# Optimization experiments

Hardware: AMD Instinct MI355X
Metric: run time of the kernel (lower is better)

## Reference

```python
import jax, jax.numpy as jnp
import numpy as np

FEAT_DIM = 2048
HID = 256
N = 1024
NUM_CLASSES = 16
BN_EPS = 1e-5


def _batchnorm(x, gamma, beta):
    # training-mode BatchNorm1d: per-batch mean, biased variance
    m = x.mean(axis=0)
    v = x.var(axis=0)
    return gamma * (x - m) / jnp.sqrt(v + BN_EPS) + beta


def setup_inputs() -> dict:
    key = jax.random.key(0)
    ks = jax.random.split(key, 12)
    s1 = 1.0 / np.sqrt(FEAT_DIM)
    s2 = 1.0 / np.sqrt(HID)
    s3 = 1.0 / np.sqrt(2 * HID)
    return {
        "features": jax.random.normal(ks[0], (N, FEAT_DIM), dtype=jnp.float32),
        "labels": jax.random.randint(ks[1], (N,), 0, NUM_CLASSES, dtype=jnp.int32),
        # semantic disentangler
        "W1": jax.random.normal(ks[2], (FEAT_DIM, HID), dtype=jnp.float32) * s1,
        "b1": jnp.zeros((HID,), jnp.float32),
        "g1": jnp.ones((HID,), jnp.float32),
        "bt1": jnp.zeros((HID,), jnp.float32),
        "W2": jax.random.normal(ks[3], (HID, HID), dtype=jnp.float32) * s2,
        "b2": jnp.zeros((HID,), jnp.float32),
        "g2": jnp.ones((HID,), jnp.float32),
        "bt2": jnp.zeros((HID,), jnp.float32),
        # edge network: Linear(2H -> H), Linear(H -> 1)
        "We1": jax.random.normal(ks[4], (2 * HID, HID), dtype=jnp.float32) * s3,
        "bwe1": jnp.zeros((HID,), jnp.float32),
        "We2": jax.random.normal(ks[5], (HID, 1), dtype=jnp.float32) * s2,
        "bwe2": jnp.zeros((1,), jnp.float32),
    }


def reference(features, labels, W1, b1, g1, bt1, W2, b2, g2, bt2,
              We1, bwe1, We2, bwe2):
    # semantic disentangler: (Linear -> BN -> ReLU) x2
    h = jax.nn.relu(_batchnorm(features @ W1 + b1, g1, bt1))
    di = jax.nn.relu(_batchnorm(h @ W2 + b2, g2, bt2))  # [N, H]

    # EdgeNetwork all-pairs: Linear on concat([f_i, f_j]) splits into two GEMMs
    hi = di @ We1[:HID]   # [N, H] contribution of node i (first half of concat)
    hj = di @ We1[HID:]   # [N, H] contribution of node j (second half)
    pair = jax.nn.relu(hi[:, None, :] + hj[None, :, :] + bwe1)  # [N, N, H]
    logits = pair @ We2[:, 0] + bwe2[0]                          # [N, N]
    same_label = labels[:, None] == labels[None, :]
    off_diag = ~jnp.eye(N, dtype=bool)
    edge_weights = jnp.where(same_label & off_diag,
                             jax.nn.sigmoid(logits), 0.0)        # [N, N]

    # update_node_features: f_i + sum_j w_ij f_j / sum_j w_ij (if wsum > 0)
    weighted_sum = edge_weights @ di                 # [N, H] (w_ii == 0)
    wsum = edge_weights.sum(axis=1, keepdims=True)   # [N, 1]
    denom = jnp.where(wsum > 0, wsum, 1.0)
    updated = di + jnp.where(wsum > 0, weighted_sum / denom, 0.0)
    return updated
```

## Files before the change

### kernel.cpp

```cpp
#include <hip/hip_runtime.h>
#include <math.h>

#define N_PTS 1024
#define HID   256
#define FEAT  2048

typedef short bf16x8 __attribute__((ext_vector_type(8)));
typedef float f32x4  __attribute__((ext_vector_type(4)));

__device__ inline ushort f2bf(float f) {
    union { float f; unsigned u; } v; v.f = f;
    unsigned r = v.u + 0x7fff + ((v.u >> 16) & 1);
    return (ushort)(r >> 16);
}

__global__ __launch_bounds__(256) void gemm_mfma(
    const float* __restrict__ A, const float* __restrict__ B,
    float* __restrict__ C, int lda, int ldb, int ldc, int kchunk)
{
    __shared__ ushort As[64 * 72];
    __shared__ ushort Bs[64 * 72];
    const int tid  = threadIdx.x;
    const int lane = tid & 63;
    const int wave = tid >> 6;
    const int wy = wave >> 1, wx = wave & 1;
    const int quad = lane >> 4, l16 = lane & 15;
    const int mBase = blockIdx.y * 64;
    const int nBase = blockIdx.x * 64;
    const int kBeg  = blockIdx.z * kchunk;

    f32x4 acc[2][2] = {};

    for (int ks = kBeg; ks < kBeg + kchunk; ks += 64) {
        #pragma unroll
        for (int p = 0; p < 4; p++) {
            const int c  = p * 256 + tid;
            const int r  = c >> 4;
            const int cq = c & 15;
            float4 av = *(const float4*)&A[(size_t)(mBase + r) * lda + ks + cq * 4];
            ushort4 ao;
            ao.x = f2bf(av.x); ao.y = f2bf(av.y);
            ao.z = f2bf(av.z); ao.w = f2bf(av.w);
            *(ushort4*)&As[r * 72 + cq * 4] = ao;
            float4 bv = *(const float4*)&B[(size_t)(ks + r) * ldb + nBase + cq * 4];
            Bs[(cq * 4 + 0) * 72 + r] = f2bf(bv.x);
            Bs[(cq * 4 + 1) * 72 + r] = f2bf(bv.y);
            Bs[(cq * 4 + 2) * 72 + r] = f2bf(bv.z);
            Bs[(cq * 4 + 3) * 72 + r] = f2bf(bv.w);
        }
        __syncthreads();
        #pragma unroll
        for (int kt = 0; kt < 64; kt += 32) {
            bf16x8 af[2], bfr[2];
            #pragma unroll
            for (int mi = 0; mi < 2; mi++)
                af[mi] = *(bf16x8*)&As[(wy * 32 + mi * 16 + l16) * 72 + kt + quad * 8];
            #pragma unroll
            for (int ni = 0; ni < 2; ni++)
                bfr[ni] = *(bf16x8*)&Bs[(wx * 32 + ni * 16 + l16) * 72 + kt + quad * 8];
            #pragma unroll
            for (int mi = 0; mi < 2; mi++)
                #pragma unroll
                for (int ni = 0; ni < 2; ni++)
                    acc[mi][ni] = __builtin_amdgcn_mfma_f32_16x16x32_bf16(
                        af[mi], bfr[ni], acc[mi][ni], 0, 0, 0);
        }
        __syncthreads();
    }
    #pragma unroll
    for (int mi = 0; mi < 2; mi++)
        #pragma unroll
        for (int ni = 0; ni < 2; ni++)
            #pragma unroll
            for (int e = 0; e < 4; e++) {
                const int gm = mBase + wy * 32 + mi * 16 + quad * 4 + e;
                const int gn = nBase + wx * 32 + ni * 16 + l16;
                unsafeAtomicAdd(&C[(size_t)gm * ldc + gn], acc[mi][ni][e]);
            }
}

__global__ __launch_bounds__(256) void colstats(
    const float* __restrict__ X, float* __restrict__ sum,
    float* __restrict__ sq, int rowsPerBlock)
{
    const int c = threadIdx.x;
    const int r0 = blockIdx.x * rowsPerBlock;
    float s = 0.f, q = 0.f;
    for (int r = r0; r < r0 + rowsPerBlock; ++r) {
        float v = X[r * HID + c];
        s += v;
        q = fmaf(v, v, q);
    }
    unsafeAtomicAdd(&sum[c], s);
    unsafeAtomicAdd(&sq[c], q);
}

__global__ __launch_bounds__(256) void bn_relu(
    const float* __restrict__ X, const float* __restrict__ sum,
    const float* __restrict__ sq, const float* __restrict__ g,
    const float* __restrict__ bt, float* __restrict__ Y)
{
    const int idx = blockIdx.x * 256 + threadIdx.x;
    const int cq = (idx & 63) * 4;
    float4 x = ((const float4*)X)[idx];
    float xv[4] = {x.x, x.y, x.z, x.w};
    float o[4];
    #pragma unroll
    for (int e = 0; e < 4; e++) {
        const int c = cq + e;
        float m   = sum[c] * (1.f / 1024.f);
        float var = fmaf(-m, m, sq[c] * (1.f / 1024.f));
        float rstd = rsqrtf(var + 1e-5f);
        o[e] = fmaxf(fmaf(g[c] * rstd, xv[e] - m, bt[c]), 0.f);
    }
    ((float4*)Y)[idx] = make_float4(o[0], o[1], o[2], o[3]);
}

__global__ __launch_bounds__(256) void gemm2_fused(
    const float* __restrict__ A , const float* __restrict__ B ,
    float* __restrict__ C ,
    const float* __restrict__ sum1, const float* __restrict__ sq1,
    const float* __restrict__ g1, const float* __restrict__ bt1,
    float* __restrict__ sum2, float* __restrict__ sq2)
{
    __shared__ ushort As[64 * 72];
    __shared__ ushort Bs[64 * 72];
    __shared__ float sscale[HID];
    __shared__ float sshift[HID];
    __shared__ float csum[64];
    __shared__ float csq[64];
    const int tid  = threadIdx.x;
    const int lane = tid & 63;
    const int wave = tid >> 6;
    const int wy = wave >> 1, wx = wave & 1;
    const int quad = lane >> 4, l16 = lane & 15;
    const int mBase = blockIdx.y * 64;
    const int nBase = blockIdx.x * 64;

    {
        float m   = sum1[tid] * (1.f / 1024.f);
        float var = fmaf(-m, m, sq1[tid] * (1.f / 1024.f));
        float rstd = rsqrtf(var + 1e-5f);
        float sc = g1[tid] * rstd;
        sscale[tid] = sc;
        sshift[tid] = fmaf(-m, sc, bt1[tid]);
    }
    if (tid < 64) { csum[tid] = 0.f; csq[tid] = 0.f; }
    __syncthreads();

    f32x4 acc[2][2] = {};
    for (int ks = 0; ks < HID; ks += 64) {
        #pragma unroll
        for (int p = 0; p < 4; p++) {
            const int c  = p * 256 + tid;
            const int r  = c >> 4;
            const int cq = c & 15;
            const int k0 = ks + cq * 4;
            float4 av = *(const float4*)&A[(size_t)(mBase + r) * HID + k0];
            float v0 = fmaxf(fmaf(sscale[k0 + 0], av.x, sshift[k0 + 0]), 0.f);
            float v1 = fmaxf(fmaf(sscale[k0 + 1], av.y, sshift[k0 + 1]), 0.f);
            float v2 = fmaxf(fmaf(sscale[k0 + 2], av.z, sshift[k0 + 2]), 0.f);
            float v3 = fmaxf(fmaf(sscale[k0 + 3], av.w, sshift[k0 + 3]), 0.f);
            ushort4 ao;
            ao.x = f2bf(v0); ao.y = f2bf(v1); ao.z = f2bf(v2); ao.w = f2bf(v3);
            *(ushort4*)&As[r * 72 + cq * 4] = ao;
            float4 bv = *(const float4*)&B[(size_t)(ks + r) * HID + nBase + cq * 4];
            Bs[(cq * 4 + 0) * 72 + r] = f2bf(bv.x);
            Bs[(cq * 4 + 1) * 72 + r] = f2bf(bv.y);
            Bs[(cq * 4 + 2) * 72 + r] = f2bf(bv.z);
            Bs[(cq * 4 + 3) * 72 + r] = f2bf(bv.w);
        }
        __syncthreads();
        #pragma unroll
        for (int kt = 0; kt < 64; kt += 32) {
            bf16x8 af[2], bfr[2];
            #pragma unroll
            for (int mi = 0; mi < 2; mi++)
                af[mi] = *(bf16x8*)&As[(wy * 32 + mi * 16 + l16) * 72 + kt + quad * 8];
            #pragma unroll
            for (int ni = 0; ni < 2; ni++)
                bfr[ni] = *(bf16x8*)&Bs[(wx * 32 + ni * 16 + l16) * 72 + kt + quad * 8];
            #pragma unroll
            for (int mi = 0; mi < 2; mi++)
                #pragma unroll
                for (int ni = 0; ni < 2; ni++)
                    acc[mi][ni] = __builtin_amdgcn_mfma_f32_16x16x32_bf16(
                        af[mi], bfr[ni], acc[mi][ni], 0, 0, 0);
        }
        __syncthreads();
    }

    float s[2] = {0.f, 0.f}, q[2] = {0.f, 0.f};
    #pragma unroll
    for (int mi = 0; mi < 2; mi++)
        #pragma unroll
        for (int ni = 0; ni < 2; ni++)
            #pragma unroll
            for (int e = 0; e < 4; e++) {
                const int gm = mBase + wy * 32 + mi * 16 + quad * 4 + e;
                const int gn = nBase + wx * 32 + ni * 16 + l16;
                float v = acc[mi][ni][e];
                C[(size_t)gm * HID + gn] = v;
                s[ni] += v;
                q[ni] = fmaf(v, v, q[ni]);
            }
    #pragma unroll
    for (int ni = 0; ni < 2; ni++) {
        float sv = s[ni], qv = q[ni];
        sv += __shfl_xor(sv, 16, 64); sv += __shfl_xor(sv, 32, 64);
        qv += __shfl_xor(qv, 16, 64); qv += __shfl_xor(qv, 32, 64);
        if (quad == 0) {
            atomicAdd(&csum[wx * 32 + ni * 16 + l16], sv);
            atomicAdd(&csq [wx * 32 + ni * 16 + l16], qv);
        }
    }
    __syncthreads();
    if (tid < 64) {
        unsafeAtomicAdd(&sum2[nBase + tid], csum[tid]);
        unsafeAtomicAdd(&sq2 [nBase + tid], csq[tid]);
    }
}

__global__ __launch_bounds__(256) void gemm_dual(
    const float* __restrict__ A, const float* __restrict__ B1,
    const float* __restrict__ B2, float* __restrict__ C1, float* __restrict__ C2)
{
    __shared__ ushort As[64 * 72];
    __shared__ ushort Bs[64 * 72];
    const int tid  = threadIdx.x;
    const int lane = tid & 63;
    const int wave = tid >> 6;
    const int wy = wave >> 1, wx = wave & 1;
    const int quad = lane >> 4, l16 = lane & 15;
    const int mBase = blockIdx.y * 64;
    const int nBase = blockIdx.x * 64;
    const float* B = (blockIdx.z >= 4) ? B2 : B1;
    float*       C = (blockIdx.z >= 4) ? C2 : C1;
    const int ks = (blockIdx.z & 3) * 64;

    f32x4 acc[2][2] = {};
    #pragma unroll
    for (int p = 0; p < 4; p++) {
        const int c  = p * 256 + tid;
        const int r  = c >> 4;
        const int cq = c & 15;
        float4 av = *(const float4*)&A[(size_t)(mBase + r) * HID + ks + cq * 4];
        ushort4 ao;
        ao.x = f2bf(av.x); ao.y = f2bf(av.y);
        ao.z = f2bf(av.z); ao.w = f2bf(av.w);
        *(ushort4*)&As[r * 72 + cq * 4] = ao;
        float4 bv = *(const float4*)&B[(size_t)(ks + r) * HID + nBase + cq * 4];
        Bs[(cq * 4 + 0) * 72 + r] = f2bf(bv.x);
        Bs[(cq * 4 + 1) * 72 + r] = f2bf(bv.y);
        Bs[(cq * 4 + 2) * 72 + r] = f2bf(bv.z);
        Bs[(cq * 4 + 3) * 72 + r] = f2bf(bv.w);
    }
    __syncthreads();
    #pragma unroll
    for (int kt = 0; kt < 64; kt += 32) {
        bf16x8 af[2], bfr[2];
        #pragma unroll
        for (int mi = 0; mi < 2; mi++)
            af[mi] = *(bf16x8*)&As[(wy * 32 + mi * 16 + l16) * 72 + kt + quad * 8];
        #pragma unroll
        for (int ni = 0; ni < 2; ni++)
            bfr[ni] = *(bf16x8*)&Bs[(wx * 32 + ni * 16 + l16) * 72 + kt + quad * 8];
        #pragma unroll
        for (int mi = 0; mi < 2; mi++)
            #pragma unroll
            for (int ni = 0; ni < 2; ni++)
                acc[mi][ni] = __builtin_amdgcn_mfma_f32_16x16x32_bf16(
                    af[mi], bfr[ni], acc[mi][ni], 0, 0, 0);
    }
    #pragma unroll
    for (int mi = 0; mi < 2; mi++)
        #pragma unroll
        for (int ni = 0; ni < 2; ni++)
            #pragma unroll
            for (int e = 0; e < 4; e++) {
                const int gm = mBase + wy * 32 + mi * 16 + quad * 4 + e;
                const int gn = nBase + wx * 32 + ni * 16 + l16;
                unsafeAtomicAdd(&C[(size_t)gm * HID + gn], acc[mi][ni][e]);
            }
}

__global__ __launch_bounds__(256) void pair_update2(
    const float* __restrict__ di, const float* __restrict__ hi,
    const float* __restrict__ hj, const float* __restrict__ bwe1,
    const float* __restrict__ We2, const float* __restrict__ bwe2,
    const int* __restrict__ labels, float* __restrict__ out)
{
    __shared__ int   slab[N_PTS];
    __shared__ int   list[N_PTS];
    __shared__ int   cnt;
    __shared__ float sacc[16][HID];
    __shared__ float swsum[16];
    const int i   = blockIdx.x;
    const int tid = threadIdx.x;
    const int pid = tid >> 4;
    const int l16 = tid & 15;

    if (tid == 0) cnt = 0;
    for (int t = tid; t < N_PTS; t += 256) slab[t] = labels[t];
    __syncthreads();
    const int myLab = slab[i];
    for (int t = tid; t < N_PTS; t += 256)
        if (slab[t] == myLab && t != i) list[atomicAdd(&cnt, 1)] = t;
    __syncthreads();
    const int n = cnt;

    const float4* hip4 = (const float4*)(hi + (size_t)i * HID) + l16 * 4;
    const float4* bw4  = (const float4*)bwe1 + l16 * 4;
    const float4* w24  = (const float4*)We2  + l16 * 4;
    float4 hb[4], w2[4];
    #pragma unroll
    for (int s = 0; s < 4; s++) {
        float4 a = hip4[s], b = bw4[s];
        hb[s] = make_float4(a.x + b.x, a.y + b.y, a.z + b.z, a.w + b.w);
        w2[s] = w24[s];
    }
    const float b2 = bwe2[0];

    float4 acc[4] = {};
    float wloc = 0.f;
    const int rounds = (n + 15) >> 4;
    for (int r = 0; r < rounds; ++r) {
        const int idx = r * 16 + pid;
        const bool valid = idx < n;
        const int jj = valid ? list[idx] : i;
        const float4* hv4 = (const float4*)(hj + (size_t)jj * HID) + l16 * 4;
        float4 hv[4];
        #pragma unroll
        for (int s = 0; s < 4; s++) hv[s] = hv4[s];
        float p = 0.f;
        #pragma unroll
        for (int s = 0; s < 4; s++) {
            p = fmaf(fmaxf(hb[s].x + hv[s].x, 0.f), w2[s].x, p);
            p = fmaf(fmaxf(hb[s].y + hv[s].y, 0.f), w2[s].y, p);
            p = fmaf(fmaxf(hb[s].z + hv[s].z, 0.f), w2[s].z, p);
            p = fmaf(fmaxf(hb[s].w + hv[s].w, 0.f), w2[s].w, p);
        }
        p += __shfl_xor(p, 1, 64);
        p += __shfl_xor(p, 2, 64);
        p += __shfl_xor(p, 4, 64);
        p += __shfl_xor(p, 8, 64);
        const float w = valid ? 1.f / (1.f + expf(-(p + b2))) : 0.f;
        const float4* dv4 = (const float4*)(di + (size_t)jj * HID) + l16 * 4;
        #pragma unroll
        for (int s = 0; s < 4; s++) {
            float4 d = dv4[s];
            acc[s].x = fmaf(w, d.x, acc[s].x);
            acc[s].y = fmaf(w, d.y, acc[s].y);
            acc[s].z = fmaf(w, d.z, acc[s].z);
            acc[s].w = fmaf(w, d.w, acc[s].w);
        }
        if (l16 == 0) wloc += w;
    }
    #pragma unroll
    for (int s = 0; s < 4; s++)
        ((float4*)&sacc[pid][l16 * 16])[s] = acc[s];
    if (l16 == 0) swsum[pid] = wloc;
    __syncthreads();

    float at = 0.f;
    #pragma unroll
    for (int g = 0; g < 16; g++) at += sacc[g][tid];
    float wt = 0.f;
    #pragma unroll
    for (int g = 0; g < 16; g++) wt += swsum[g];
    const float dval = di[(size_t)i * HID + tid];
    out[(size_t)i * HID + tid] = dval + (wt > 0.f ? at / wt : 0.f);
}

extern "C" void kernel_launch(void* const* d_in, const int* in_sizes, int n_in,
                              void* d_out, int out_size, void* d_ws, size_t ws_size,
                              hipStream_t stream)
{
    const float* features = (const float*)d_in[0];
    const int*   labels   = (const int*)d_in[1];
    const float* W1   = (const float*)d_in[2];
    const float* g1   = (const float*)d_in[4];
    const float* bt1  = (const float*)d_in[5];
    const float* W2   = (const float*)d_in[6];
    const float* g2   = (const float*)d_in[8];
    const float* bt2  = (const float*)d_in[9];
    const float* We1  = (const float*)d_in[10];
    const float* bwe1 = (const float*)d_in[11];
    const float* We2  = (const float*)d_in[12];
    const float* bwe2 = (const float*)d_in[13];
    float* out = (float*)d_out;

    float* ws    = (float*)d_ws;
    float* x1    = ws;
    float* hi    = ws + 262144;
    float* hj    = ws + 524288;
    float* stats = ws + 786432;
    float* x2    = ws + 787456;
    float* di    = ws + 1049600;

    hipMemsetAsync(d_ws, 0, 787456 * sizeof(float), stream);

    dim3 blk(256);
    gemm_mfma<<<dim3(4, 16, 8), blk, 0, stream>>>(features, W1, x1,
                                                  FEAT, HID, HID, 256);
    colstats<<<256, blk, 0, stream>>>(x1, stats, stats + 256, 4);
    gemm2_fused<<<dim3(4, 16, 1), blk, 0, stream>>>(x1, W2, x2,
                                                    stats, stats + 256, g1, bt1,
                                                    stats + 512, stats + 768);
    bn_relu<<<256, blk, 0, stream>>>(x2, stats + 512, stats + 768, g2, bt2, di);
    gemm_dual<<<dim3(4, 16, 8), blk, 0, stream>>>(di, We1, We1 + HID * HID,
                                                  hi, hj);
    pair_update2<<<N_PTS, blk, 0, stream>>>(di, hi, hj, bwe1, We2, bwe2,
                                            labels, out);
}
```

Before: 155.1 us.

## Pre-convert inputs and weights to transposed bf16 and fuse BN2 into dual GEMM

```diff
diff --git a/kernel.cpp b/kernel.cpp
--- a/kernel.cpp
+++ b/kernel.cpp
@@ -14,8 +14,61 @@
     return (ushort)(r >> 16);
 }
 
-__global__ __launch_bounds__(256) void gemm_mfma(
-    const float* __restrict__ A, const float* __restrict__ B,
+__global__ __launch_bounds__(256) void prep(
+    const float* __restrict__ features, const float* __restrict__ W1,
+    const float* __restrict__ W2, const float* __restrict__ We1,
+    ushort* __restrict__ Af, ushort* __restrict__ W1T,
+    ushort* __restrict__ W2T, ushort* __restrict__ WeT)
+{
+    const int tid = threadIdx.x;
+    int b = blockIdx.x;
+    if (b < 512) {
+        #pragma unroll
+        for (int q = 0; q < 2; q++) {
+            const size_t g = (size_t)b * 256 + tid + (size_t)q * 131072;
+            float4 v0 = ((const float4*)features)[g * 2];
+            float4 v1 = ((const float4*)features)[g * 2 + 1];
+            bf16x8 o;
+            o[0] = (short)f2bf(v0.x); o[1] = (short)f2bf(v0.y);
+            o[2] = (short)f2bf(v0.z); o[3] = (short)f2bf(v0.w);
+            o[4] = (short)f2bf(v1.x); o[5] = (short)f2bf(v1.y);
+            o[6] = (short)f2bf(v1.z); o[7] = (short)f2bf(v1.w);
+            ((bf16x8*)Af)[g] = o;
+        }
+        return;
+    }
+    __shared__ ushort Ts[64 * 72];
+    const float* src; ushort* dst; int K;
+    b -= 512;
+    if (b < 128)      { src = W1;  dst = W1T; K = 2048; }
+    else if (b < 144) { b -= 128; src = W2;  dst = W2T; K = 256; }
+    else              { b -= 144; src = We1; dst = WeT; K = 512; }
+    const int k0 = (b >> 2) * 64;
+    const int n0 = (b & 3) * 64;
+    #pragma unroll
+    for (int p = 0; p < 4; p++) {
+        const int c  = p * 256 + tid;
+        const int r  = c >> 4;
+        const int cq = c & 15;
+        float4 v = *(const float4*)&src[(size_t)(k0 + r) * 256 + n0 + cq * 4];
+        Ts[(cq * 4 + 0) * 72 + r] = f2bf(v.x);
+        Ts[(cq * 4 + 1) * 72 + r] = f2bf(v.y);
+        Ts[(cq * 4 + 2) * 72 + r] = f2bf(v.z);
+        Ts[(cq * 4 + 3) * 72 + r] = f2bf(v.w);
+    }
+    __syncthreads();
+    #pragma unroll
+    for (int p = 0; p < 2; p++) {
+        const int c    = p * 256 + tid;
+        const int row  = c >> 3;
+        const int col8 = c & 7;
+        *(bf16x8*)&dst[(size_t)(n0 + row) * K + k0 + col8 * 8] =
+            *(bf16x8*)&Ts[row * 72 + col8 * 8];
+    }
+}
+
+__global__ __launch_bounds__(256) void gemm_bf(
+    const ushort* __restrict__ A, const ushort* __restrict__ B,
     float* __restrict__ C, int lda, int ldb, int ldc, int kchunk)
 {
     __shared__ ushort As[64 * 72];
@@ -30,23 +83,16 @@
     const int kBeg  = blockIdx.z * kchunk;
 
     f32x4 acc[2][2] = {};
-
     for (int ks = kBeg; ks < kBeg + kchunk; ks += 64) {
         #pragma unroll
-        for (int p = 0; p < 4; p++) {
-            const int c  = p * 256 + tid;
-            const int r  = c >> 4;
-            const int cq = c & 15;
-            float4 av = *(const float4*)&A[(size_t)(mBase + r) * lda + ks + cq * 4];
-            ushort4 ao;
-            ao.x = f2bf(av.x); ao.y = f2bf(av.y);
-            ao.z = f2bf(av.z); ao.w = f2bf(av.w);
-            *(ushort4*)&As[r * 72 + cq * 4] = ao;
-            float4 bv = *(const float4*)&B[(size_t)(ks + r) * ldb + nBase + cq * 4];
-            Bs[(cq * 4 + 0) * 72 + r] = f2bf(bv.x);
-            Bs[(cq * 4 + 1) * 72 + r] = f2bf(bv.y);
-            Bs[(cq * 4 + 2) * 72 + r] = f2bf(bv.z);
-            Bs[(cq * 4 + 3) * 72 + r] = f2bf(bv.w);
+        for (int p = 0; p < 2; p++) {
+            const int c    = p * 256 + tid;
+            const int row  = c >> 3;
+            const int col8 = c & 7;
+            *(bf16x8*)&As[row * 72 + col8 * 8] =
+                *(const bf16x8*)&A[(size_t)(mBase + row) * lda + ks + col8 * 8];
+            *(bf16x8*)&Bs[row * 72 + col8 * 8] =
+                *(const bf16x8*)&B[(size_t)(nBase + row) * ldb + ks + col8 * 8];
         }
         __syncthreads();
         #pragma unroll
@@ -95,29 +141,8 @@
     unsafeAtomicAdd(&sq[c], q);
 }
 
-__global__ __launch_bounds__(256) void bn_relu(
-    const float* __restrict__ X, const float* __restrict__ sum,
-    const float* __restrict__ sq, const float* __restrict__ g,
-    const float* __restrict__ bt, float* __restrict__ Y)
-{
-    const int idx = blockIdx.x * 256 + threadIdx.x;
-    const int cq = (idx & 63) * 4;
-    float4 x = ((const float4*)X)[idx];
-    float xv[4] = {x.x, x.y, x.z, x.w};
-    float o[4];
-    #pragma unroll
-    for (int e = 0; e < 4; e++) {
-        const int c = cq + e;
-        float m   = sum[c] * (1.f / 1024.f);
-        float var = fmaf(-m, m, sq[c] * (1.f / 1024.f));
-        float rstd = rsqrtf(var + 1e-5f);
-        o[e] = fmaxf(fmaf(g[c] * rstd, xv[e] - m, bt[c]), 0.f);
-    }
-    ((float4*)Y)[idx] = make_float4(o[0], o[1], o[2], o[3]);
-}
-
 __global__ __launch_bounds__(256) void gemm2_fused(
-    const float* __restrict__ A , const float* __restrict__ B ,
+    const float* __restrict__ A , const ushort* __restrict__ B ,
     float* __restrict__ C ,
     const float* __restrict__ sum1, const float* __restrict__ sq1,
     const float* __restrict__ g1, const float* __restrict__ bt1,
@@ -164,11 +189,14 @@
             ushort4 ao;
             ao.x = f2bf(v0); ao.y = f2bf(v1); ao.z = f2bf(v2); ao.w = f2bf(v3);
             *(ushort4*)&As[r * 72 + cq * 4] = ao;
-            float4 bv = *(const float4*)&B[(size_t)(ks + r) * HID + nBase + cq * 4];
-            Bs[(cq * 4 + 0) * 72 + r] = f2bf(bv.x);
-            Bs[(cq * 4 + 1) * 72 + r] = f2bf(bv.y);
-            Bs[(cq * 4 + 2) * 72 + r] = f2bf(bv.z);
-            Bs[(cq * 4 + 3) * 72 + r] = f2bf(bv.w);
+        }
+        #pragma unroll
+        for (int p = 0; p < 2; p++) {
+            const int c    = p * 256 + tid;
+            const int row  = c >> 3;
+            const int col8 = c & 7;
+            *(bf16x8*)&Bs[row * 72 + col8 * 8] =
+                *(const bf16x8*)&B[(size_t)(nBase + row) * HID + ks + col8 * 8];
         }
         __syncthreads();
         #pragma unroll
@@ -221,12 +249,17 @@
     }
 }
 
-__global__ __launch_bounds__(256) void gemm_dual(
-    const float* __restrict__ A, const float* __restrict__ B1,
-    const float* __restrict__ B2, float* __restrict__ C1, float* __restrict__ C2)
+__global__ __launch_bounds__(256) void gemm_dual_bn(
+    const float* __restrict__ A , const ushort* __restrict__ WeT,
+    float* __restrict__ C1 , float* __restrict__ C2 ,
+    const float* __restrict__ sum2, const float* __restrict__ sq2,
+    const float* __restrict__ g2, const float* __restrict__ bt2,
+    float* __restrict__ di)
 {
     __shared__ ushort As[64 * 72];
     __shared__ ushort Bs[64 * 72];
+    __shared__ float sscale[HID];
+    __shared__ float sshift[HID];
     const int tid  = threadIdx.x;
     const int lane = tid & 63;
     const int wave = tid >> 6;
@@ -234,28 +267,50 @@
     const int quad = lane >> 4, l16 = lane & 15;
     const int mBase = blockIdx.y * 64;
     const int nBase = blockIdx.x * 64;
-    const float* B = (blockIdx.z >= 4) ? B2 : B1;
-    float*       C = (blockIdx.z >= 4) ? C2 : C1;
-    const int ks = (blockIdx.z & 3) * 64;
-
-    f32x4 acc[2][2] = {};
+    const int half  = blockIdx.z >> 2;
+    const int ks    = (blockIdx.z & 3) * 64;
+    float* C = half ? C2 : C1;
+    const bool writeDi = (blockIdx.x == 0) && (half == 0);
+
+    {
+        float m   = sum2[tid] * (1.f / 1024.f);
+        float var = fmaf(-m, m, sq2[tid] * (1.f / 1024.f));
+        float rstd = rsqrtf(var + 1e-5f);
+        float sc = g2[tid] * rstd;
+        sscale[tid] = sc;
+        sshift[tid] = fmaf(-m, sc, bt2[tid]);
+    }
+    __syncthreads();
+
     #pragma unroll
     for (int p = 0; p < 4; p++) {
         const int c  = p * 256 + tid;
         const int r  = c >> 4;
         const int cq = c & 15;
-        float4 av = *(const float4*)&A[(size_t)(mBase + r) * HID + ks + cq * 4];
+        const int k0 = ks + cq * 4;
+        float4 av = *(const float4*)&A[(size_t)(mBase + r) * HID + k0];
+        float v0 = fmaxf(fmaf(sscale[k0 + 0], av.x, sshift[k0 + 0]), 0.f);
+        float v1 = fmaxf(fmaf(sscale[k0 + 1], av.y, sshift[k0 + 1]), 0.f);
+        float v2 = fmaxf(fmaf(sscale[k0 + 2], av.z, sshift[k0 + 2]), 0.f);
+        float v3 = fmaxf(fmaf(sscale[k0 + 3], av.w, sshift[k0 + 3]), 0.f);
+        if (writeDi)
+            *(float4*)&di[(size_t)(mBase + r) * HID + k0] =
+                make_float4(v0, v1, v2, v3);
         ushort4 ao;
-        ao.x = f2bf(av.x); ao.y = f2bf(av.y);
-        ao.z = f2bf(av.z); ao.w = f2bf(av.w);
+        ao.x = f2bf(v0); ao.y = f2bf(v1); ao.z = f2bf(v2); ao.w = f2bf(v3);
         *(ushort4*)&As[r * 72 + cq * 4] = ao;
-        float4 bv = *(const float4*)&B[(size_t)(ks + r) * HID + nBase + cq * 4];
-        Bs[(cq * 4 + 0) * 72 + r] = f2bf(bv.x);
-        Bs[(cq * 4 + 1) * 72 + r] = f2bf(bv.y);
-        Bs[(cq * 4 + 2) * 72 + r] = f2bf(bv.z);
-        Bs[(cq * 4 + 3) * 72 + r] = f2bf(bv.w);
-    }
-    __syncthreads();
+    }
+    #pragma unroll
+    for (int p = 0; p < 2; p++) {
+        const int c    = p * 256 + tid;
+        const int row  = c >> 3;
+        const int col8 = c & 7;
+        *(bf16x8*)&Bs[row * 72 + col8 * 8] =
+            *(const bf16x8*)&WeT[(size_t)(nBase + row) * 512 + half * 256 + ks + col8 * 8];
+    }
+    __syncthreads();
+
+    f32x4 acc[2][2] = {};
     #pragma unroll
     for (int kt = 0; kt < 64; kt += 32) {
         bf16x8 af[2], bfr[2];
@@ -397,19 +452,24 @@
     float* stats = ws + 786432;
     float* x2    = ws + 787456;
     float* di    = ws + 1049600;
+    ushort* Af   = (ushort*)(ws + 1311744);
+    ushort* W1T  = Af + 2097152;
+    ushort* W2T  = W1T + 524288;
+    ushort* WeT  = W2T + 65536;
 
     hipMemsetAsync(d_ws, 0, 787456 * sizeof(float), stream);
 
     dim3 blk(256);
-    gemm_mfma<<<dim3(4, 16, 8), blk, 0, stream>>>(features, W1, x1,
-                                                  FEAT, HID, HID, 256);
+    prep<<<688, blk, 0, stream>>>(features, W1, W2, We1, Af, W1T, W2T, WeT);
+    gemm_bf<<<dim3(4, 16, 8), blk, 0, stream>>>(Af, W1T, x1,
+                                                FEAT, FEAT, HID, 256);
     colstats<<<256, blk, 0, stream>>>(x1, stats, stats + 256, 4);
-    gemm2_fused<<<dim3(4, 16, 1), blk, 0, stream>>>(x1, W2, x2,
+    gemm2_fused<<<dim3(4, 16, 1), blk, 0, stream>>>(x1, W2T, x2,
                                                     stats, stats + 256, g1, bt1,
                                                     stats + 512, stats + 768);
-    bn_relu<<<256, blk, 0, stream>>>(x2, stats + 512, stats + 768, g2, bt2, di);
-    gemm_dual<<<dim3(4, 16, 8), blk, 0, stream>>>(di, We1, We1 + HID * HID,
-                                                  hi, hj);
+    gemm_dual_bn<<<dim3(4, 16, 8), blk, 0, stream>>>(x2, WeT, hi, hj,
+                                                     stats + 512, stats + 768,
+                                                     g2, bt2, di);
     pair_update2<<<N_PTS, blk, 0, stream>>>(di, hi, hj, bwe1, We2, bwe2,
                                             labels, out);
 }
```

Measured after the change: 145.4 us. 1.07x faster.
